# Optimization experiments

Hardware: AMD Instinct MI355X
Metric: run time of the kernel (lower is better)

## Reference

```python
import jax, jax.numpy as jnp
import numpy as np

B = 4
DIM = 512          # d_model
L = 4096           # n_tokens
D_STATE = 16
D_CONV = 4
EXPAND = 2
D_INNER = EXPAND * DIM          # 1024
DT_RANK = (DIM + 15) // 16      # ceil(dim/16) = 32
EPS = 1e-5


def setup_inputs() -> dict:
    key = jax.random.key(0)
    ks = jax.random.split(key, 8)
    s = 0.02
    A_log = jnp.log(jnp.tile(jnp.arange(1.0, D_STATE + 1.0, dtype=jnp.float32), (D_INNER, 1)))
    return {
        "x": jax.random.normal(ks[0], (B, DIM, L), jnp.float32),
        "ln_w": jnp.ones((DIM,), jnp.float32),
        "ln_b": jnp.zeros((DIM,), jnp.float32),
        "W_in": jax.random.normal(ks[1], (2 * D_INNER, DIM), jnp.float32) * s,
        "conv_w": jax.random.normal(ks[2], (D_INNER, 1, D_CONV), jnp.float32) * s,
        "conv_b": jnp.zeros((D_INNER,), jnp.float32),
        "W_xproj": jax.random.normal(ks[3], (DT_RANK + 2 * D_STATE, D_INNER), jnp.float32) * s,
        "W_dt": jax.random.normal(ks[4], (D_INNER, DT_RANK), jnp.float32) * s,
        "b_dt": jax.random.normal(ks[5], (D_INNER,), jnp.float32) * 0.1,
        "A_log": A_log,
        "D": jnp.ones((D_INNER,), jnp.float32),
        "W_out": jax.random.normal(ks[6], (DIM, D_INNER), jnp.float32) * s,
    }


def reference(x, ln_w, ln_b, W_in, conv_w, conv_b, W_xproj, W_dt, b_dt, A_log, D, W_out):
    Bsz = x.shape[0]
    # [B, d_model, L] -> [B, L, d_model]
    xt = jnp.swapaxes(x, 1, 2)
    # LayerNorm
    mu = jnp.mean(xt, axis=-1, keepdims=True)
    var = jnp.mean(jnp.square(xt - mu), axis=-1, keepdims=True)
    xn = (xt - mu) * jax.lax.rsqrt(var + EPS) * ln_w + ln_b
    # in_proj -> x, z branches
    xz = xn @ W_in.T                       # [B, L, 2*d_inner]
    xin, z = jnp.split(xz, 2, axis=-1)
    # causal depthwise conv1d (torch pads d_conv-1 both sides then truncates to L)
    xc = jnp.swapaxes(xin, 1, 2)           # [B, d_inner, L]
    xc = jax.lax.conv_general_dilated(
        xc, conv_w, window_strides=(1,), padding=[(D_CONV - 1, 0)],
        dimension_numbers=("NCH", "OIH", "NCH"), feature_group_count=D_INNER)
    xc = xc + conv_b[None, :, None]
    u = jax.nn.silu(jnp.swapaxes(xc, 1, 2))  # [B, L, d_inner]
    # input-dependent SSM parameters
    dbl = u @ W_xproj.T                    # [B, L, dt_rank + 2*d_state]
    dt = dbl[..., :DT_RANK]
    Bm = dbl[..., DT_RANK:DT_RANK + D_STATE]
    Cm = dbl[..., DT_RANK + D_STATE:]
    delta = jax.nn.softplus(dt @ W_dt.T + b_dt)  # [B, L, d_inner]
    A = -jnp.exp(A_log)                    # [d_inner, d_state]

    def step(h, inp):
        d_t, b_t, c_t, u_t = inp           # [B,di], [B,ds], [B,ds], [B,di]
        dA = jnp.exp(d_t[..., None] * A)   # [B, di, ds]
        h = dA * h + (d_t * u_t)[..., None] * b_t[:, None, :]
        y = jnp.einsum("bds,bs->bd", h, c_t)
        return h, y

    h0 = jnp.zeros((Bsz, D_INNER, D_STATE), x.dtype)
    xs = (jnp.swapaxes(delta, 0, 1), jnp.swapaxes(Bm, 0, 1),
          jnp.swapaxes(Cm, 0, 1), jnp.swapaxes(u, 0, 1))
    _, ys = jax.lax.scan(step, h0, xs)     # ys: [L, B, d_inner]
    y = jnp.swapaxes(ys, 0, 1) + u * D
    y = y * jax.nn.silu(z)
    out = y @ W_out.T                      # [B, L, d_model]
    return jnp.swapaxes(out, 1, 2)         # [B, d_model, L]
```

## Files before the change

### kernel.cpp

```cpp
#include <hip/hip_runtime.h>
#include <math.h>

#define Bsz 4
#define DIM 512
#define LEN 4096
#define DST 16
#define DIN 1024
#define NCH 64
#define CHL 64

typedef unsigned short ushort_t;
typedef unsigned int uint_t;
typedef __attribute__((ext_vector_type(8))) short short8;
typedef __attribute__((ext_vector_type(8))) unsigned short ushort8;
typedef __attribute__((ext_vector_type(8))) _Float16 half8;
typedef __attribute__((ext_vector_type(4))) float f32x4;

__device__ __forceinline__ float sigmoidf_(float x){ return 1.0f/(1.0f+__expf(-x)); }
__device__ __forceinline__ float bf2f(ushort_t u){ return __uint_as_float(((uint_t)u) << 16); }
__device__ __forceinline__ ushort_t f2bf(float f){
  uint_t x = __float_as_uint(f);
  uint_t r = (x + 0x7FFFu + ((x >> 16) & 1u)) >> 16;
  return (ushort_t)r;
}
__device__ __forceinline__ ushort_t f2h_bits(float f){
  _Float16 h = (_Float16)f;
  union { _Float16 h; ushort_t u; } v; v.h = h; return v.u;
}
__device__ __forceinline__ void gl2lds16(const void* g, void* l){
  __builtin_amdgcn_global_load_lds((const __attribute__((address_space(1))) void*)g,
                                   (__attribute__((address_space(3))) void*)l, 16, 0, 0);
}
#define POW_CHAIN(av, a1) \
  { float a2=a1*a1, a4=a2*a2, a8=a4*a4; \
    av[0]=a1; av[1]=a2; av[2]=a2*a1; av[3]=a4; \
    av[4]=a4*a1; av[5]=a4*a2; av[6]=a4*av[2]; av[7]=a8; \
    av[8]=a8*a1; av[9]=a8*a2; av[10]=a8*av[2]; av[11]=a8*a4; \
    av[12]=a8*av[4]; av[13]=a8*av[5]; av[14]=a8*av[6]; av[15]=a8*a8; }

__device__ __forceinline__ bool load_nA(const float* Alog, int d, float* nA){
  bool fast = true;
  #pragma unroll
  for(int s=0;s<DST;s++){
    float v = -__expf(Alog[d*DST+s]);
    float tgt = -(float)(s+1);
    if(fabsf(v - tgt) < 1e-4f*(float)(s+1)) v = tgt;
    else fast = false;
    nA[s] = v;
  }
  return fast;
}

__global__ __launch_bounds__(256) void ln_stats_k(const float* __restrict__ x,
                                                  float* __restrict__ mu, float* __restrict__ rs){
  int bid = blockIdx.x;
  int b = bid >> 6;
  int lg = bid & 63;
  int lane = threadIdx.x & 63;
  int g = threadIdx.x >> 6;
  int l = lg*64 + lane;
  const float* xb = x + (size_t)b*DIM*LEN + l;
  float s = 0.f, sq = 0.f;
  for(int d = g*128; d < g*128 + 128; ++d){
    float v = xb[(size_t)d*LEN];
    s += v; sq += v*v;
  }
  __shared__ float rsum[4][64], rsq[4][64];
  rsum[g][lane] = s; rsq[g][lane] = sq;
  __syncthreads();
  if(threadIdx.x < 64){
    float ts = 0.f, tq = 0.f;
    for(int gg=0; gg<4; ++gg){ ts += rsum[gg][lane]; tq += rsq[gg][lane]; }
    float m = ts * (1.0f/DIM);
    float var = tq * (1.0f/DIM) - m*m;
    mu[b*LEN + l] = m;
    rs[b*LEN + l] = rsqrtf(var + 1e-5f);
  }
}

__global__ __launch_bounds__(256) void wcvt_k(const float* __restrict__ Win,
    const float* __restrict__ Wout, const float* __restrict__ Wxp,
    ushort_t* __restrict__ Winb, ushort_t* __restrict__ Woutb, ushort_t* __restrict__ Wxpb){
  int i = blockIdx.x*256 + threadIdx.x;
  if(i < 1048576) Winb[i] = f2bf(Win[i]);
  else if(i < 1572864) Woutb[i-1048576] = f2bf(Wout[i-1048576]);
  else if(i < 1638400) Wxpb[i-1572864] = f2bf(Wxp[i-1572864]);
}

__global__ __launch_bounds__(256) void xnt_k(const float* __restrict__ x,
    const float* __restrict__ mu, const float* __restrict__ rs,
    const float* __restrict__ lnw, const float* __restrict__ lnb, ushort_t* __restrict__ xnT){
  __shared__ ushort_t t[64][72];
  int bid = blockIdx.x;
  int lt = bid & 63;
  int dt_ = (bid >> 6) & 7;
  int b = bid >> 9;
  int l0 = lt*64, d0 = dt_*64;
  int ll = threadIdx.x & 63;
  int dq = threadIdx.x >> 6;
  float mul_ = mu[b*LEN + l0 + ll], rsl = rs[b*LEN + l0 + ll];
  const float* xb = x + (size_t)b*DIM*LEN;
  #pragma unroll
  for(int i=0;i<16;i++){
    int d = d0 + dq*16 + i;
    float v = xb[(size_t)d*LEN + l0 + ll];
    t[ll][dq*16 + i] = f2bf((v - mul_)*rsl*lnw[d] + lnb[d]);
  }
  __syncthreads();
  int lr = threadIdx.x >> 2, seg = threadIdx.x & 3;
  ushort_t* dst = &xnT[(size_t)(b*LEN + l0 + lr)*DIM + d0 + seg*16];
  #pragma unroll
  for(int k=0;k<4;k++){
    ushort4 v = *(const ushort4*)&t[lr][seg*16 + k*4];
    *(ushort4*)&dst[k*4] = v;
  }
}

__global__ __launch_bounds__(256) void gemm1_mfma(const ushort_t* __restrict__ A,
    const ushort_t* __restrict__ Bw, _Float16* __restrict__ xin, ushort_t* __restrict__ sz){
  __shared__ __align__(16) ushort_t smem[2*16384];
  int tid = threadIdx.x;
  int wave = tid >> 6, lane = tid & 63;
  int flat = blockIdx.y * 16 + blockIdx.x;
  int orig = (flat & 7) * 256 + (flat >> 3);
  int n0 = (orig & 15) * 128;
  int m0 = (orig >> 4) * 128;
  int wm = (wave >> 1) * 64, wn = (wave & 1) * 64;
  int lm = lane & 15;
  int lk = lane >> 4;
  int sx = lm & 7;
  f32x4 zero4 = {0.f,0.f,0.f,0.f};
  f32x4 acc[4][4];
  #pragma unroll
  for(int i=0;i<4;i++)
    #pragma unroll
    for(int j=0;j<4;j++) acc[i][j] = zero4;
  #pragma unroll
  for(int i=0;i<4;i++){
    int c = i*256 + tid, r = c >> 3, kc = c & 7;
    int kg = kc ^ (r & 7);
    gl2lds16(&A [(size_t)(m0 + r)*512 + kg*8], &smem[c*8]);
    gl2lds16(&Bw[(size_t)(n0 + r)*512 + kg*8], &smem[8192 + c*8]);
  }
  __syncthreads();
  int cur = 0;
  for(int t=0; t<8; ++t){
    if(t < 7){
      int k0n = (t+1)*64;
      ushort_t* Ad = &smem[(cur^1)*16384];
      ushort_t* Bd = &smem[(cur^1)*16384 + 8192];
      #pragma unroll
      for(int i=0;i<4;i++){
        int c = i*256 + tid, r = c >> 3, kc = c & 7;
        int kg = kc ^ (r & 7);
        gl2lds16(&A [(size_t)(m0 + r)*512 + k0n + kg*8], &Ad[c*8]);
        gl2lds16(&Bw[(size_t)(n0 + r)*512 + k0n + kg*8], &Bd[c*8]);
      }
    }
    const ushort_t* As = &smem[cur*16384];
    const ushort_t* Bs = &smem[cur*16384 + 8192];
    #pragma unroll
    for(int kk=0; kk<64; kk+=32){
      short8 af[4], bf[4];
      int ch = ((kk >> 3) + lk) ^ sx;
      #pragma unroll
      for(int i=0;i<4;i++){
        af[i] = *(const short8*)&As[(wm + i*16 + lm)*64 + ch*8];
        bf[i] = *(const short8*)&Bs[(wn + i*16 + lm)*64 + ch*8];
      }
      #pragma unroll
      for(int i=0;i<4;i++)
        #pragma unroll
        for(int j=0;j<4;j++)
          acc[i][j] = __builtin_amdgcn_mfma_f32_16x16x32_bf16(af[i], bf[j], acc[i][j], 0, 0, 0);
    }
    __syncthreads();
    cur ^= 1;
  }
  ushort_t* T = smem;
  bool is_z = (n0 >= 1024);
  #pragma unroll
  for(int i=0;i<4;i++)
    #pragma unroll
    for(int j=0;j<4;j++)
      #pragma unroll
      for(int r=0;r<4;r++){
        int ml = wm + i*16 + lk*4 + r;
        int nl = wn + j*16 + lm;
        float v = acc[i][j][r];
        T[ml*136 + nl] = is_z ? f2bf(v * sigmoidf_(v)) : f2h_bits(v);
      }
  __syncthreads();
  int rr = tid >> 4, cc = (tid & 15)*8;
  #pragma unroll
  for(int p=0;p<8;p++){
    int row = p*16 + rr;
    ushort8 v = *(const ushort8*)&T[row*136 + cc];
    if(!is_z) *(ushort8*)((ushort_t*)xin + (size_t)(m0+row)*DIN + n0 + cc) = v;
    else      *(ushort8*)&sz[(size_t)(m0+row)*DIN + (n0-1024) + cc] = v;
  }
}

__global__ __launch_bounds__(256) void conv_silu_k(const _Float16* __restrict__ xin,
    const float* __restrict__ cw, const float* __restrict__ cb, ushort_t* __restrict__ u){
  int idx = blockIdx.x*256 + threadIdx.x;
  int dg = idx & 127;
  int lc = (idx >> 7) & 511;
  int b  = idx >> 16;
  int d0 = dg*8;
  int l0 = lc*8;
  float bias[8];
  #pragma unroll
  for(int k=0;k<8;k+=4){
    float4 c4 = *(const float4*)&cb[d0+k];
    bias[k]=c4.x; bias[k+1]=c4.y; bias[k+2]=c4.z; bias[k+3]=c4.w;
  }
  float w[8][4];
  #pragma unroll
  for(int k=0;k<8;k++){
    float4 c4 = *(const float4*)&cw[(d0+k)*4];
    w[k][0]=c4.x; w[k][1]=c4.y; w[k][2]=c4.z; w[k][3]=c4.w;
  }
  const _Float16* base = xin + ((size_t)b*LEN)*DIN + d0;
  ushort_t* ub = u + ((size_t)b*LEN)*DIN + d0;
  float f0[8], f1[8], f2[8];
  if(lc > 0){
    half8 h0 = *(const half8*)&base[(size_t)(l0-3)*DIN];
    half8 h1 = *(const half8*)&base[(size_t)(l0-2)*DIN];
    half8 h2 = *(const half8*)&base[(size_t)(l0-1)*DIN];
    #pragma unroll
    for(int k=0;k<8;k++){ f0[k]=(float)h0[k]; f1[k]=(float)h1[k]; f2[k]=(float)h2[k]; }
  } else {
    #pragma unroll
    for(int k=0;k<8;k++){ f0[k]=0.f; f1[k]=0.f; f2[k]=0.f; }
  }
  #pragma unroll
  for(int t=0;t<8;t++){
    half8 xv = *(const half8*)&base[(size_t)(l0+t)*DIN];
    float f3[8];
    #pragma unroll
    for(int k=0;k<8;k++) f3[k] = (float)xv[k];
    short8 o;
    #pragma unroll
    for(int k=0;k<8;k++){
      float a = bias[k] + f0[k]*w[k][0] + f1[k]*w[k][1] + f2[k]*w[k][2] + f3[k]*w[k][3];
      float v = a * sigmoidf_(a);
      o[k] = (short)f2bf(v);
    }
    *(short8*)&ub[(size_t)(l0+t)*DIN] = o;
    #pragma unroll
    for(int k=0;k<8;k++){ f0[k]=f1[k]; f1[k]=f2[k]; f2[k]=f3[k]; }
  }
}

__global__ __launch_bounds__(256) void gemm2_mfma(const ushort_t* __restrict__ A,
    const ushort_t* __restrict__ Bw, float* __restrict__ dbl){
  __shared__ __align__(16) ushort_t smem[2*12288];
  int tid = threadIdx.x;
  int wave = tid >> 6, lane = tid & 63;
  int m0 = blockIdx.x * 128;
  int wm = (wave >> 1) * 64, wn = (wave & 1) * 32;
  int lm = lane & 15;
  int lk = lane >> 4;
  int sx = lm & 7;
  f32x4 zero4 = {0.f,0.f,0.f,0.f};
  f32x4 acc[4][2];
  #pragma unroll
  for(int i=0;i<4;i++){ acc[i][0] = zero4; acc[i][1] = zero4; }
  #pragma unroll
  for(int i=0;i<4;i++){
    int c = i*256 + tid, r = c >> 3, kc = c & 7;
    int kg = kc ^ (r & 7);
    gl2lds16(&A[(size_t)(m0 + r)*1024 + kg*8], &smem[c*8]);
  }
  #pragma unroll
  for(int i=0;i<2;i++){
    int c = i*256 + tid, r = c >> 3, kc = c & 7;
    int kg = kc ^ (r & 7);
    gl2lds16(&Bw[(size_t)r*1024 + kg*8], &smem[8192 + c*8]);
  }
  __syncthreads();
  int cur = 0;
  for(int t=0; t<16; ++t){
    if(t < 15){
      int k0n = (t+1)*64;
      ushort_t* Ad = &smem[(cur^1)*12288];
      ushort_t* Bd = &smem[(cur^1)*12288 + 8192];
      #pragma unroll
      for(int i=0;i<4;i++){
        int c = i*256 + tid, r = c >> 3, kc = c & 7;
        int kg = kc ^ (r & 7);
        gl2lds16(&A[(size_t)(m0 + r)*1024 + k0n + kg*8], &Ad[c*8]);
      }
      #pragma unroll
      for(int i=0;i<2;i++){
        int c = i*256 + tid, r = c >> 3, kc = c & 7;
        int kg = kc ^ (r & 7);
        gl2lds16(&Bw[(size_t)r*1024 + k0n + kg*8], &Bd[c*8]);
      }
    }
    const ushort_t* As = &smem[cur*12288];
    const ushort_t* Bs = &smem[cur*12288 + 8192];
    #pragma unroll
    for(int kk=0; kk<64; kk+=32){
      short8 af[4], bf[2];
      int ch = ((kk >> 3) + lk) ^ sx;
      #pragma unroll
      for(int i=0;i<4;i++) af[i] = *(const short8*)&As[(wm + i*16 + lm)*64 + ch*8];
      #pragma unroll
      for(int j=0;j<2;j++) bf[j] = *(const short8*)&Bs[(wn + j*16 + lm)*64 + ch*8];
      #pragma unroll
      for(int i=0;i<4;i++)
        #pragma unroll
        for(int j=0;j<2;j++)
          acc[i][j] = __builtin_amdgcn_mfma_f32_16x16x32_bf16(af[i], bf[j], acc[i][j], 0, 0, 0);
    }
    __syncthreads();
    cur ^= 1;
  }
  #pragma unroll
  for(int i=0;i<4;i++)
    #pragma unroll
    for(int j=0;j<2;j++)
      #pragma unroll
      for(int r=0;r<4;r++){
        int m = m0 + wm + i*16 + lk*4 + r;
        int n = wn + j*16 + lm;
        dbl[(size_t)m*64 + n] = acc[i][j][r];
      }
}

__global__ __launch_bounds__(256,4) void deltag_k(const float* __restrict__ dbl,
    const float* __restrict__ Wdt, const float* __restrict__ bdt,
    _Float16* __restrict__ dF){
  __shared__ __align__(16) float dts[64*32];
  int bid = blockIdx.x;
  int d0 = (bid & 3) * 256;
  int m0 = (bid >> 2) * 64;
  int tid = threadIdx.x;
  const f32x4* src4 = (const f32x4*)(dbl + (size_t)m0*64);
  f32x4* dst4 = (f32x4*)dts;
  for(int i=tid; i<64*8; i+=256){
    int row = i >> 3, q = i & 7;
    dst4[i] = src4[row*16 + q];
  }
  int d = d0 + tid;
  float w[32];
  #pragma unroll
  for(int k=0;k<32;k+=4){
    float4 t4 = *(const float4*)&Wdt[d*32+k];
    w[k]=t4.x; w[k+1]=t4.y; w[k+2]=t4.z; w[k+3]=t4.w;
  }
  float bd = bdt[d];
  __syncthreads();
  for(int m=0;m<64;m++){
    const float* row = dts + m*32;
    float dtv = bd;
    #pragma unroll
    for(int k=0;k<32;k+=4){
      f32x4 q = *(const f32x4*)&row[k];
      dtv += q.x*w[k] + q.y*w[k+1] + q.z*w[k+2] + q.w*w[k+3];
    }
    float dv = dtv > 15.f ? dtv : __logf(1.f + __expf(dtv));
    dF[(size_t)(m0+m)*DIN + d] = (_Float16)dv;
  }
}

__global__ __launch_bounds__(256,4) void scanA_k(const ushort_t* __restrict__ u,
    const float* __restrict__ dbl, const float* __restrict__ Alog,
    const _Float16* __restrict__ dF,
    float* __restrict__ E, float* __restrict__ cum){
  __shared__ __align__(16) float dch[CHL*16];
  int bid = blockIdx.x;
  int c = bid & (NCH-1);
  int dblk = (bid >> 6) & 3;
  int b = bid >> 8;
  int d = dblk*256 + threadIdx.x;
  const f32x4* src = (const f32x4*)(dbl + ((size_t)b*LEN + c*CHL)*64);
  f32x4* dst4 = (f32x4*)dch;
  for(int i=threadIdx.x; i<CHL*4; i+=256){
    int t = i >> 2, q = i & 3;
    dst4[i] = src[t*16 + 8 + q];
  }
  float nA[DST];
  bool fast = load_nA(Alog, d, nA);
  float Es[DST];
  #pragma unroll
  for(int s=0;s<DST;s++) Es[s] = 0.f;
  float cumD = 0.f;
  __syncthreads();
  const ushort_t*  uu = u  + ((size_t)b*LEN + c*CHL)*DIN + d;
  const _Float16*  pd = dF + ((size_t)b*LEN + c*CHL)*DIN + d;
  if(fast){
    for(int t=0;t<CHL;++t){
      float dv = (float)pd[(size_t)t*DIN];
      float uv = bf2f(uu[(size_t)t*DIN]);
      float du = dv*uv;
      cumD += dv;
      float a1 = __expf(-dv);
      float av[DST];
      POW_CHAIN(av, a1);
      const f32x4* r4 = (const f32x4*)(dch + t*16);
      f32x4 B0=r4[0], B1=r4[1], B2=r4[2], B3=r4[3];
      Es[0]=av[0]*Es[0]+du*B0.x;  Es[1]=av[1]*Es[1]+du*B0.y;
      Es[2]=av[2]*Es[2]+du*B0.z;  Es[3]=av[3]*Es[3]+du*B0.w;
      Es[4]=av[4]*Es[4]+du*B1.x;  Es[5]=av[5]*Es[5]+du*B1.y;
      Es[6]=av[6]*Es[6]+du*B1.z;  Es[7]=av[7]*Es[7]+du*B1.w;
      Es[8]=av[8]*Es[8]+du*B2.x;  Es[9]=av[9]*Es[9]+du*B2.y;
      Es[10]=av[10]*Es[10]+du*B2.z; Es[11]=av[11]*Es[11]+du*B2.w;
      Es[12]=av[12]*Es[12]+du*B3.x; Es[13]=av[13]*Es[13]+du*B3.y;
      Es[14]=av[14]*Es[14]+du*B3.z; Es[15]=av[15]*Es[15]+du*B3.w;
    }
  } else {
    for(int t=0;t<CHL;++t){
      float dv = (float)pd[(size_t)t*DIN];
      float uv = bf2f(uu[(size_t)t*DIN]);
      float du = dv*uv;
      cumD += dv;
      const float* row = dch + t*16;
      #pragma unroll
      for(int s=0;s<DST;s++){
        float a = __expf(dv*nA[s]);
        Es[s] = a*Es[s] + du*row[s];
      }
    }
  }
  size_t o = (size_t)(b*NCH + c)*DST*DIN + d;
  #pragma unroll
  for(int s=0;s<DST;s++) E[o + (size_t)s*DIN] = Es[s];
  cum[(size_t)(b*NCH + c)*DIN + d] = cumD;
}

__global__ __launch_bounds__(256) void scanB_k(const float* __restrict__ cum,
    const float* __restrict__ Alog, float* __restrict__ E){
  int g = blockIdx.x*256 + threadIdx.x;
  int d = g & 1023;
  int s = (g >> 10) & 15;
  int b = g >> 14;
  float v = -__expf(Alog[d*DST + s]);
  float tgt = -(float)(s+1);
  float nA = (fabsf(v - tgt) < 1e-4f*(float)(s+1)) ? tgt : v;
  float h = 0.f;
  for(int c=0;c<NCH;c++){
    float p = __expf(cum[(size_t)(b*NCH + c)*DIN + d] * nA);
    size_t o = (size_t)((b*NCH + c)*DST + s)*DIN + d;
    float e = E[o];
    E[o] = h;
    h = p*h + e;
  }
}

__global__ __launch_bounds__(256,4) void scanC_k(ushort_t* __restrict__ u,
    const float* __restrict__ dbl, const float* __restrict__ Alog,
    const float* __restrict__ Hs, const float* __restrict__ Dp, const ushort_t* __restrict__ sz,
    const _Float16* __restrict__ dF){
  __shared__ __align__(16) float dch[CHL*32];
  int bid = blockIdx.x;
  int c = bid & (NCH-1);
  int dblk = (bid >> 6) & 3;
  int b = bid >> 8;
  int d = dblk*256 + threadIdx.x;
  const f32x4* src = (const f32x4*)(dbl + ((size_t)b*LEN + c*CHL)*64);
  f32x4* dst4 = (f32x4*)dch;
  for(int i=threadIdx.x; i<CHL*8; i+=256){
    int t = i >> 3, q = i & 7;
    dst4[i] = src[t*16 + 8 + q];
  }
  float nA[DST];
  bool fast = load_nA(Alog, d, nA);
  float h[DST];
  size_t ho = (size_t)(b*NCH + c)*DST*DIN + d;
  #pragma unroll
  for(int s=0;s<DST;s++) h[s] = Hs[ho + (size_t)s*DIN];
  float Dv = Dp[d];
  __syncthreads();
  ushort_t* uu = u + ((size_t)b*LEN + c*CHL)*DIN + d;
  const ushort_t* zz = sz + ((size_t)b*LEN + c*CHL)*DIN + d;
  const _Float16* pd = dF + ((size_t)b*LEN + c*CHL)*DIN + d;
  if(fast){
    for(int t=0;t<CHL;++t){
      float dv = (float)pd[(size_t)t*DIN];
      float uv = bf2f(uu[(size_t)t*DIN]);
      float du = dv*uv;
      float a1 = __expf(-dv);
      float av[DST];
      POW_CHAIN(av, a1);
      const f32x4* r4 = (const f32x4*)(dch + t*32);
      f32x4 B0=r4[0], B1=r4[1], B2=r4[2], B3=r4[3];
      f32x4 C0=r4[4], C1=r4[5], C2=r4[6], C3=r4[7];
      float y0, y1, y2, y3;
      h[0]=av[0]*h[0]+du*B0.x;  h[1]=av[1]*h[1]+du*B0.y;
      h[2]=av[2]*h[2]+du*B0.z;  h[3]=av[3]*h[3]+du*B0.w;
      y0 = h[0]*C0.x + h[1]*C0.y; y1 = h[2]*C0.z + h[3]*C0.w;
      h[4]=av[4]*h[4]+du*B1.x;  h[5]=av[5]*h[5]+du*B1.y;
      h[6]=av[6]*h[6]+du*B1.z;  h[7]=av[7]*h[7]+du*B1.w;
      y2 = h[4]*C1.x + h[5]*C1.y; y3 = h[6]*C1.z + h[7]*C1.w;
      h[8]=av[8]*h[8]+du*B2.x;  h[9]=av[9]*h[9]+du*B2.y;
      h[10]=av[10]*h[10]+du*B2.z; h[11]=av[11]*h[11]+du*B2.w;
      y0 += h[8]*C2.x + h[9]*C2.y; y1 += h[10]*C2.z + h[11]*C2.w;
      h[12]=av[12]*h[12]+du*B3.x; h[13]=av[13]*h[13]+du*B3.y;
      h[14]=av[14]*h[14]+du*B3.z; h[15]=av[15]*h[15]+du*B3.w;
      y2 += h[12]*C3.x + h[13]*C3.y; y3 += h[14]*C3.z + h[15]*C3.w;
      float y = (y0+y1) + (y2+y3) + uv*Dv;
      y *= bf2f(zz[(size_t)t*DIN]);
      uu[(size_t)t*DIN] = f2bf(y);
    }
  } else {
    for(int t=0;t<CHL;++t){
      float dv = (float)pd[(size_t)t*DIN];
      float uv = bf2f(uu[(size_t)t*DIN]);
      float du = dv*uv;
      const float* row = dch + t*32;
      float y = 0.f;
      #pragma unroll
      for(int s=0;s<DST;s++){
        float a = __expf(dv*nA[s]);
        h[s] = a*h[s] + du*row[s];
        y += h[s]*row[16+s];
      }
      y += uv*Dv;
      y *= bf2f(zz[(size_t)t*DIN]);
      uu[(size_t)t*DIN] = f2bf(y);
    }
  }
}

__global__ __launch_bounds__(256) void gemm4_mfma(const ushort_t* __restrict__ A,
    const ushort_t* __restrict__ Bw, float* __restrict__ out){
  __shared__ __align__(16) ushort_t smem[2*16384];
  int tid = threadIdx.x;
  int wave = tid >> 6, lane = tid & 63;
  int flat = blockIdx.y * 4 + blockIdx.x;
  int orig = (flat & 7) * 64 + (flat >> 3);
  int n0 = (orig & 3) * 128;
  int m0 = (orig >> 2) * 128;
  int wm = (wave >> 1) * 64, wn = (wave & 1) * 64;
  int lm = lane & 15;
  int lk = lane >> 4;
  int sx = lm & 7;
  f32x4 zero4 = {0.f,0.f,0.f,0.f};
  f32x4 acc[4][4];
  #pragma unroll
  for(int i=0;i<4;i++)
    #pragma unroll
    for(int j=0;j<4;j++) acc[i][j] = zero4;
  #pragma unroll
  for(int i=0;i<4;i++){
    int c = i*256 + tid, r = c >> 3, kc = c & 7;
    int kg = kc ^ (r & 7);
    gl2lds16(&A [(size_t)(m0 + r)*1024 + kg*8], &smem[c*8]);
    gl2lds16(&Bw[(size_t)(n0 + r)*1024 + kg*8], &smem[8192 + c*8]);
  }
  __syncthreads();
  int cur = 0;
  for(int t=0; t<16; ++t){
    if(t < 15){
      int k0n = (t+1)*64;
      ushort_t* Ad = &smem[(cur^1)*16384];
      ushort_t* Bd = &smem[(cur^1)*16384 + 8192];
      #pragma unroll
      for(int i=0;i<4;i++){
        int c = i*256 + tid, r = c >> 3, kc = c & 7;
        int kg = kc ^ (r & 7);
        gl2lds16(&A [(size_t)(m0 + r)*1024 + k0n + kg*8], &Ad[c*8]);
        gl2lds16(&Bw[(size_t)(n0 + r)*1024 + k0n + kg*8], &Bd[c*8]);
      }
    }
    const ushort_t* As = &smem[cur*16384];
    const ushort_t* Bs = &smem[cur*16384 + 8192];
    #pragma unroll
    for(int kk=0; kk<64; kk+=32){
      short8 af[4], bf[4];
      int ch = ((kk >> 3) + lk) ^ sx;
      #pragma unroll
      for(int i=0;i<4;i++){
        af[i] = *(const short8*)&As[(wm + i*16 + lm)*64 + ch*8];
        bf[i] = *(const short8*)&Bs[(wn + i*16 + lm)*64 + ch*8];
      }
      #pragma unroll
      for(int i=0;i<4;i++)
        #pragma unroll
        for(int j=0;j<4;j++)
          acc[i][j] = __builtin_amdgcn_mfma_f32_16x16x32_bf16(af[i], bf[j], acc[i][j], 0, 0, 0);
    }
    __syncthreads();
    cur ^= 1;
  }
  float* T = (float*)smem;
  int b = m0 >> 12, l0 = m0 & 4095;
  for(int g=0; g<4; ++g){
    __syncthreads();
    if((g >> 1) == (wave & 1)){
      int jg = g & 1;
      #pragma unroll
      for(int j2=0;j2<2;j2++){
        int j = jg*2 + j2;
        #pragma unroll
        for(int i=0;i<4;i++)
          #pragma unroll
          for(int r=0;r<4;r++){
            int ml = wm + i*16 + lk*4 + r;
            int nl = wn + j*16 + lm - g*32;
            T[nl*132 + ml] = acc[i][j][r];
          }
      }
    }
    __syncthreads();
    int nl = tid >> 3, seg = tid & 7;
    float* dst = &out[((size_t)b*DIM + n0 + g*32 + nl)*LEN + l0 + seg*16];
    #pragma unroll
    for(int k=0;k<4;k++){
      float4 v = *(const float4*)&T[nl*132 + seg*16 + k*4];
      *(float4*)&dst[k*4] = v;
    }
  }
}

extern "C" void kernel_launch(void* const* d_in, const int* in_sizes, int n_in,
                              void* d_out, int out_size, void* d_ws, size_t ws_size,
                              hipStream_t stream) {
  const float* x    = (const float*)d_in[0];
  const float* lnw  = (const float*)d_in[1];
  const float* lnb  = (const float*)d_in[2];
  const float* Win  = (const float*)d_in[3];
  const float* cw   = (const float*)d_in[4];
  const float* cb   = (const float*)d_in[5];
  const float* Wxp  = (const float*)d_in[6];
  const float* Wdt  = (const float*)d_in[7];
  const float* bdt  = (const float*)d_in[8];
  const float* Alog = (const float*)d_in[9];
  const float* Dp   = (const float*)d_in[10];
  const float* Wout = (const float*)d_in[11];
  float* out = (float*)d_out;
  float* ws  = (float*)d_ws;

  float*    mu   = ws;
  float*    rs   = ws + 16384;
  _Float16* xin  = (_Float16*)(ws + 32768);
  _Float16* dF   = (_Float16*)(ws + 32768);
  float*    E    = ws + 32768 + 8388608;
  float*    cum  = ws + 32768 + 12582912;
  ushort_t* sz   = (ushort_t*)(ws + 32768 + 16777216);
  ushort_t* u    = (ushort_t*)(ws + 32768 + 16777216 + 8388608);
  ushort_t* xnT  = (ushort_t*)(ws + 32768 + 16777216 + 16777216);
  float*    dbl  = (float*)xnT;
  ushort_t* Winb = (ushort_t*)(ws + 32768 + 16777216 + 16777216 + 4194304);
  ushort_t* Woutb= Winb + 1048576;
  ushort_t* Wxpb = Woutb + 524288;

  hipLaunchKernelGGL(ln_stats_k, dim3(256),     dim3(256), 0, stream, x, mu, rs);
  hipLaunchKernelGGL(wcvt_k,     dim3(6400),    dim3(256), 0, stream, Win, Wout, Wxp, Winb, Woutb, Wxpb);
  hipLaunchKernelGGL(xnt_k,      dim3(2048),    dim3(256), 0, stream, x, mu, rs, lnw, lnb, xnT);
  hipLaunchKernelGGL(gemm1_mfma, dim3(16,128),  dim3(256), 0, stream, xnT, Winb, xin, sz);
  hipLaunchKernelGGL(conv_silu_k,dim3(1024),    dim3(256), 0, stream, xin, cw, cb, u);
  hipLaunchKernelGGL(gemm2_mfma, dim3(128),     dim3(256), 0, stream, u, Wxpb, dbl);
  hipLaunchKernelGGL(deltag_k,   dim3(1024),    dim3(256), 0, stream, dbl, Wdt, bdt, dF);
  hipLaunchKernelGGL(scanA_k,    dim3(1024),    dim3(256), 0, stream, u, dbl, Alog, dF, E, cum);
  hipLaunchKernelGGL(scanB_k,    dim3(256),     dim3(256), 0, stream, cum, Alog, E);
  hipLaunchKernelGGL(scanC_k,    dim3(1024),    dim3(256), 0, stream, u, dbl, Alog, E, Dp, sz, dF);
  hipLaunchKernelGGL(gemm4_mfma, dim3(4,128),   dim3(256), 0, stream, u, Woutb, out);
}
```

Measured before the change: 350.4 us.

## Use partial vmcnt waits in GEMM pipelines and halve gemm2 row tile

In the three MFMA GEMMs, the full __syncthreads after each prefetch is replaced by an s_waitcnt that waits only for the current stage's global-to-LDS loads, followed by a raw s_barrier. The aim is to let the next tile's loads stay in flight while the current tile is computed. Separately, gemm2 now uses 64-row tiles and 256 blocks instead of 128, so the skinny xproj GEMM fills more CUs. The risks are correctness if the hard-coded vmcnt counts do not match the number of issued loads, and more redundant loads of the weight tile in gemm2.

```diff
diff --git a/kernel.cpp b/kernel.cpp
--- a/kernel.cpp
+++ b/kernel.cpp
@@ -142,7 +142,6 @@
     gl2lds16(&A [(size_t)(m0 + r)*512 + kg*8], &smem[c*8]);
     gl2lds16(&Bw[(size_t)(n0 + r)*512 + kg*8], &smem[8192 + c*8]);
   }
-  __syncthreads();
   int cur = 0;
   for(int t=0; t<8; ++t){
     if(t < 7){
@@ -156,7 +155,12 @@
         gl2lds16(&A [(size_t)(m0 + r)*512 + k0n + kg*8], &Ad[c*8]);
         gl2lds16(&Bw[(size_t)(n0 + r)*512 + k0n + kg*8], &Bd[c*8]);
       }
-    }
+      asm volatile("s_waitcnt vmcnt(8)" ::: "memory");
+    } else {
+      asm volatile("s_waitcnt vmcnt(0)" ::: "memory");
+    }
+    __builtin_amdgcn_sched_barrier(0);
+    __builtin_amdgcn_s_barrier();
     const ushort_t* As = &smem[cur*16384];
     const ushort_t* Bs = &smem[cur*16384 + 8192];
     #pragma unroll
@@ -174,7 +178,7 @@
         for(int j=0;j<4;j++)
           acc[i][j] = __builtin_amdgcn_mfma_f32_16x16x32_bf16(af[i], bf[j], acc[i][j], 0, 0, 0);
     }
-    __syncthreads();
+    __builtin_amdgcn_s_barrier();
     cur ^= 1;
   }
   ushort_t* T = smem;
@@ -255,71 +259,65 @@
 
 __global__ __launch_bounds__(256) void gemm2_mfma(const ushort_t* __restrict__ A,
     const ushort_t* __restrict__ Bw, float* __restrict__ dbl){
-  __shared__ __align__(16) ushort_t smem[2*12288];
+  __shared__ __align__(16) ushort_t smem[2*8192];
   int tid = threadIdx.x;
   int wave = tid >> 6, lane = tid & 63;
-  int m0 = blockIdx.x * 128;
-  int wm = (wave >> 1) * 64, wn = (wave & 1) * 32;
+  int m0 = blockIdx.x * 64;
+  int wm = (wave >> 1) * 32, wn = (wave & 1) * 32;
   int lm = lane & 15;
   int lk = lane >> 4;
   int sx = lm & 7;
   f32x4 zero4 = {0.f,0.f,0.f,0.f};
-  f32x4 acc[4][2];
-  #pragma unroll
-  for(int i=0;i<4;i++){ acc[i][0] = zero4; acc[i][1] = zero4; }
-  #pragma unroll
-  for(int i=0;i<4;i++){
-    int c = i*256 + tid, r = c >> 3, kc = c & 7;
-    int kg = kc ^ (r & 7);
-    gl2lds16(&A[(size_t)(m0 + r)*1024 + kg*8], &smem[c*8]);
-  }
+  f32x4 acc[2][2];
+  #pragma unroll
+  for(int i=0;i<2;i++){ acc[i][0] = zero4; acc[i][1] = zero4; }
   #pragma unroll
   for(int i=0;i<2;i++){
     int c = i*256 + tid, r = c >> 3, kc = c & 7;
     int kg = kc ^ (r & 7);
-    gl2lds16(&Bw[(size_t)r*1024 + kg*8], &smem[8192 + c*8]);
-  }
-  __syncthreads();
+    gl2lds16(&A [(size_t)(m0 + r)*1024 + kg*8], &smem[c*8]);
+    gl2lds16(&Bw[(size_t)r*1024 + kg*8], &smem[4096 + c*8]);
+  }
   int cur = 0;
   for(int t=0; t<16; ++t){
     if(t < 15){
       int k0n = (t+1)*64;
-      ushort_t* Ad = &smem[(cur^1)*12288];
-      ushort_t* Bd = &smem[(cur^1)*12288 + 8192];
-      #pragma unroll
-      for(int i=0;i<4;i++){
-        int c = i*256 + tid, r = c >> 3, kc = c & 7;
-        int kg = kc ^ (r & 7);
-        gl2lds16(&A[(size_t)(m0 + r)*1024 + k0n + kg*8], &Ad[c*8]);
-      }
+      ushort_t* Ad = &smem[(cur^1)*8192];
+      ushort_t* Bd = &smem[(cur^1)*8192 + 4096];
       #pragma unroll
       for(int i=0;i<2;i++){
         int c = i*256 + tid, r = c >> 3, kc = c & 7;
         int kg = kc ^ (r & 7);
+        gl2lds16(&A [(size_t)(m0 + r)*1024 + k0n + kg*8], &Ad[c*8]);
         gl2lds16(&Bw[(size_t)r*1024 + k0n + kg*8], &Bd[c*8]);
       }
-    }
-    const ushort_t* As = &smem[cur*12288];
-    const ushort_t* Bs = &smem[cur*12288 + 8192];
+      asm volatile("s_waitcnt vmcnt(4)" ::: "memory");
+    } else {
+      asm volatile("s_waitcnt vmcnt(0)" ::: "memory");
+    }
+    __builtin_amdgcn_sched_barrier(0);
+    __builtin_amdgcn_s_barrier();
+    const ushort_t* As = &smem[cur*8192];
+    const ushort_t* Bs = &smem[cur*8192 + 4096];
     #pragma unroll
     for(int kk=0; kk<64; kk+=32){
-      short8 af[4], bf[2];
+      short8 af[2], bf[2];
       int ch = ((kk >> 3) + lk) ^ sx;
       #pragma unroll
-      for(int i=0;i<4;i++) af[i] = *(const short8*)&As[(wm + i*16 + lm)*64 + ch*8];
+      for(int i=0;i<2;i++) af[i] = *(const short8*)&As[(wm + i*16 + lm)*64 + ch*8];
       #pragma unroll
       for(int j=0;j<2;j++) bf[j] = *(const short8*)&Bs[(wn + j*16 + lm)*64 + ch*8];
       #pragma unroll
-      for(int i=0;i<4;i++)
+      for(int i=0;i<2;i++)
         #pragma unroll
         for(int j=0;j<2;j++)
           acc[i][j] = __builtin_amdgcn_mfma_f32_16x16x32_bf16(af[i], bf[j], acc[i][j], 0, 0, 0);
     }
-    __syncthreads();
+    __builtin_amdgcn_s_barrier();
     cur ^= 1;
   }
   #pragma unroll
-  for(int i=0;i<4;i++)
+  for(int i=0;i<2;i++)
     #pragma unroll
     for(int j=0;j<2;j++)
       #pragma unroll
@@ -551,7 +549,6 @@
     gl2lds16(&A [(size_t)(m0 + r)*1024 + kg*8], &smem[c*8]);
     gl2lds16(&Bw[(size_t)(n0 + r)*1024 + kg*8], &smem[8192 + c*8]);
   }
-  __syncthreads();
   int cur = 0;
   for(int t=0; t<16; ++t){
     if(t < 15){
@@ -565,7 +562,12 @@
         gl2lds16(&A [(size_t)(m0 + r)*1024 + k0n + kg*8], &Ad[c*8]);
         gl2lds16(&Bw[(size_t)(n0 + r)*1024 + k0n + kg*8], &Bd[c*8]);
       }
-    }
+      asm volatile("s_waitcnt vmcnt(8)" ::: "memory");
+    } else {
+      asm volatile("s_waitcnt vmcnt(0)" ::: "memory");
+    }
+    __builtin_amdgcn_sched_barrier(0);
+    __builtin_amdgcn_s_barrier();
     const ushort_t* As = &smem[cur*16384];
     const ushort_t* Bs = &smem[cur*16384 + 8192];
     #pragma unroll
@@ -583,7 +585,7 @@
         for(int j=0;j<4;j++)
           acc[i][j] = __builtin_amdgcn_mfma_f32_16x16x32_bf16(af[i], bf[j], acc[i][j], 0, 0, 0);
     }
-    __syncthreads();
+    __builtin_amdgcn_s_barrier();
     cur ^= 1;
   }
   float* T = (float*)smem;
@@ -653,7 +655,7 @@
   hipLaunchKernelGGL(xnt_k,      dim3(2048),    dim3(256), 0, stream, x, mu, rs, lnw, lnb, xnT);
   hipLaunchKernelGGL(gemm1_mfma, dim3(16,128),  dim3(256), 0, stream, xnT, Winb, xin, sz);
   hipLaunchKernelGGL(conv_silu_k,dim3(1024),    dim3(256), 0, stream, xin, cw, cb, u);
-  hipLaunchKernelGGL(gemm2_mfma, dim3(128),     dim3(256), 0, stream, u, Wxpb, dbl);
+  hipLaunchKernelGGL(gemm2_mfma, dim3(256),     dim3(256), 0, stream, u, Wxpb, dbl);
   hipLaunchKernelGGL(deltag_k,   dim3(1024),    dim3(256), 0, stream, dbl, Wdt, bdt, dF);
   hipLaunchKernelGGL(scanA_k,    dim3(1024),    dim3(256), 0, stream, u, dbl, Alog, dF, E, cum);
   hipLaunchKernelGGL(scanB_k,    dim3(256),     dim3(256), 0, stream, cum, Alog, E);
```

Result: no change. 353.7 us (+0.9%).
